# Performance work log

Measured on AMD Instinct MI355X. Metric: run time of the kernel, lower is better.

The kernel has to match this reference:

```python
import jax, jax.numpy as jnp
import numpy as np

N, E, C, NTT, NMOL = 200000, 1600000, 128, 20000, 2000
EPS = 1e-5


def setup_inputs() -> dict:
    key = jax.random.key(0)
    ks = jax.random.split(key, 32)
    s = 0.05
    d = {}
    d["node_attr"] = jax.random.normal(ks[0], (N, C), jnp.float32)
    d["adj_index"] = jax.random.randint(ks[1], (2, E), 0, N)
    d["adj_value"] = jax.random.uniform(ks[2], (E,), jnp.float32)
    d["tt_node_batch"] = jnp.sort(jax.random.randint(ks[3], (N,), 0, NTT))
    d["tt_graph_batch"] = jnp.sort(jax.random.randint(ks[4], (NTT,), 0, NMOL))
    # GCN layers (2): linear weight/bias
    d["W_gcn"] = jax.random.normal(ks[5], (2, C, C)) * s
    d["b_gcn"] = jnp.zeros((2, C))
    # 8 BatchNorm1d(C): [gcn0, gcn1, tt0, tt1, tt2, mol0, mol1, mol2] (eval mode)
    d["bn_gamma"] = jnp.ones((8, C))
    d["bn_beta"] = jnp.zeros((8, C))
    d["bn_mean"] = jnp.zeros((8, C))
    d["bn_var"] = jnp.ones((8, C))
    # 2 GATConv (tt, mol): bipartite lin_src/lin_dst, att_src/att_dst, bias (heads=1)
    d["gat_Wsrc"] = jax.random.normal(ks[6], (2, C, C)) * s
    d["gat_Wdst"] = jax.random.normal(ks[7], (2, C, C)) * s
    d["gat_asrc"] = jax.random.normal(ks[8], (2, C)) * s
    d["gat_adst"] = jax.random.normal(ks[9], (2, C)) * s
    d["gat_bias"] = jnp.zeros((2, C))
    # 2 GRUCell(C, C)
    d["gru_Wih"] = jax.random.normal(ks[10], (2, 3 * C, C)) * s
    d["gru_Whh"] = jax.random.normal(ks[11], (2, 3 * C, C)) * s
    d["gru_bih"] = jnp.zeros((2, 3 * C))
    d["gru_bhh"] = jnp.zeros((2, 3 * C))
    # predictor: 128 -> 64 (relu) -> 1
    d["pW1"] = jax.random.normal(ks[12], (64, C)) * s
    d["pb1"] = jnp.full((64,), 0.01)
    d["pW2"] = jax.random.normal(ks[13], (1, 64)) * s
    d["pb2"] = jnp.full((1,), 0.01)
    return d


def _bn(x, i, g, b, m, v):
    return (x - m[i]) * (g[i] / jnp.sqrt(v[i] + EPS)) + b[i]


def _spmm(idx, val, x, n):  # out[i] = sum_j A[i,j] x[j]
    return jax.ops.segment_sum(val[:, None] * x[idx[1]], idx[0], num_segments=n)


def _gat(x_src, x_dst, src, dst, nseg, Ws, Wd, a_s, a_d, bias):
    hs = x_src @ Ws.T
    hd = x_dst @ Wd.T
    alpha = jax.nn.leaky_relu(hs @ a_s, 0.01 * 0 + 0.01) if False else None
    a = (hs @ a_s)[src] + (hd @ a_d)[dst]
    a = jnp.where(a > 0, a, 0.01 * a)  # leaky_relu, negative_slope=0.01
    mx = jax.ops.segment_max(a, dst, num_segments=nseg)
    e = jnp.exp(a - mx[dst])
    den = jax.ops.segment_sum(e, dst, num_segments=nseg)
    w = e / den[dst]
    return jax.ops.segment_sum(w[:, None] * hs[src], dst, num_segments=nseg) + bias


def _gru(x, h, Wih, Whh, bih, bhh):
    gi = x @ Wih.T + bih
    gh = h @ Whh.T + bhh
    ir, iz, inn = jnp.split(gi, 3, axis=-1)
    hr, hz, hn = jnp.split(gh, 3, axis=-1)
    r = jax.nn.sigmoid(ir + hr)
    z = jax.nn.sigmoid(iz + hz)
    n = jnp.tanh(inn + r * hn)
    return (1.0 - z) * n + z * h


def _pool_stage(x, seg, nseg, bn_base, gi, bn_gamma, bn_beta, bn_mean, bn_var,
                gat_Wsrc, gat_Wdst, gat_asrc, gat_adst, gat_bias,
                gru_Wih, gru_Whh, gru_bih, gru_bhh):
    x = _bn(x, bn_base, bn_gamma, bn_beta, bn_mean, bn_var)
    mean = jax.ops.segment_sum(x, seg, num_segments=nseg)  # global_add_pool
    mean = _bn(jax.nn.relu(mean), bn_base + 1, bn_gamma, bn_beta, bn_mean, bn_var)
    src = jnp.arange(x.shape[0])
    g = _gat(x, mean, src, seg, nseg, gat_Wsrc[gi], gat_Wdst[gi], gat_asrc[gi], gat_adst[gi], gat_bias[gi])
    g = jax.nn.elu(g)  # dropout p=0.001 is identity in eval
    g = _gru(g, mean, gru_Wih[gi], gru_Whh[gi], gru_bih[gi], gru_bhh[gi])
    return _bn(jax.nn.relu(g), bn_base + 2, bn_gamma, bn_beta, bn_mean, bn_var)


def reference(node_attr, adj_value, W_gcn, b_gcn, bn_gamma, bn_beta, bn_mean, bn_var,
              gat_Wsrc, gat_Wdst, gat_asrc, gat_adst, gat_bias,
              gru_Wih, gru_Whh, gru_bih, gru_bhh, pW1, pb1, pW2, pb2,
              adj_index, tt_node_batch, tt_graph_batch):
    # graph embedder: two GCN layers  x <- relu(BN(A @ (x W^T) + b))
    x = node_attr
    for i in range(2):
        x = _spmm(adj_index, adj_value, x @ W_gcn[i].T, N) + b_gcn[i]
        x = jax.nn.relu(_bn(x, i, bn_gamma, bn_beta, bn_mean, bn_var))
    # tt pooling: nodes -> tt subgraphs
    tt = _pool_stage(x, tt_node_batch, NTT, 2, 0, bn_gamma, bn_beta, bn_mean, bn_var,
                     gat_Wsrc, gat_Wdst, gat_asrc, gat_adst, gat_bias,
                     gru_Wih, gru_Whh, gru_bih, gru_bhh)
    # mol pooling: tt subgraphs -> molecules
    mol = _pool_stage(tt, tt_graph_batch, NMOL, 5, 1, bn_gamma, bn_beta, bn_mean, bn_var,
                      gat_Wsrc, gat_Wdst, gat_asrc, gat_adst, gat_bias,
                      gru_Wih, gru_Whh, gru_bih, gru_bhh)
    # predictor
    h = jax.nn.relu(mol @ pW1.T + pb1)
    return h @ pW2.T + pb2  # [NMOL, 1]
```

## Files before the change

### kernel.cpp

```cpp
#include <hip/hip_runtime.h>
#include <math.h>

#define CCH 128
#define G3  384
#define BN_EPS 1e-5f
#define BSH 9
#define BROWS 512
#define COLBITS 19

typedef __bf16 bf16;
typedef __bf16 bf16x2 __attribute__((ext_vector_type(2)));
typedef __bf16 bf16x4 __attribute__((ext_vector_type(4)));
typedef __bf16 bf16x8 __attribute__((ext_vector_type(8)));
typedef float f32x4 __attribute__((ext_vector_type(4)));

__global__ __launch_bounds__(256) void prep_kernel(
    const float* __restrict__ g, const float* __restrict__ b,
    const float* __restrict__ m, const float* __restrict__ v,
    float* __restrict__ bnsc, float* __restrict__ bnsh,
    const float* __restrict__ Wsrc, const float* __restrict__ Wdst,
    const float* __restrict__ asrc, const float* __restrict__ adst,
    float* __restrict__ vsp, float* __restrict__ vd, float* __restrict__ c0,
    const int* __restrict__ tt_node_batch, int N, int NTT, int* __restrict__ starts_tt,
    const int* __restrict__ tt_graph_batch, int NMOL, int* __restrict__ starts_mol,
    int* __restrict__ bhist,
    const float* __restrict__ Wgcn, bf16* __restrict__ Wgcnb,
    bf16* __restrict__ Wsrcb,
    const float* __restrict__ Wih, bf16* __restrict__ Wihb,
    const float* __restrict__ Whh, bf16* __restrict__ Whhb,
    int B1, int B2, int B3, int B4, int B5, int B6, int B7, int B8)
{
    __shared__ float red[2];
    const int bid = blockIdx.x;
    const int tid = threadIdx.x;
    if (bid < B1) {
        int idx = bid * 256 + tid;
        if (idx < 8 * CCH) {
            float s = g[idx] / sqrtf(v[idx] + BN_EPS);
            bnsc[idx] = s;
            bnsh[idx] = b[idx] - m[idx] * s;
        }
    } else if (bid < B2) {
        int s = bid - B1;
        int which = tid >> 7, k = tid & 127;
        const float* W = (which ? Wdst : Wsrc) + s * CCH * CCH;
        const float* a = (which ? adst : asrc) + s * CCH;
        float acc = 0.f;
        for (int j = 0; j < CCH; ++j) acc += W[j * CCH + k] * a[j];
        if (which) {
            vd[s * CCH + k] = acc;
        } else {
            int l = 2 + 3 * s;
            float scl = g[l * CCH + k] / sqrtf(v[l * CCH + k] + BN_EPS);
            float shf = b[l * CCH + k] - m[l * CCH + k] * scl;
            vsp[s * CCH + k] = acc * scl;
            float p = shf * acc;
            for (int o = 32; o; o >>= 1) p += __shfl_down(p, o);
            if ((k & 63) == 0) red[k >> 6] = p;
        }
        __syncthreads();
        if (tid == 0) c0[s] = red[0] + red[1];
    } else if (bid < B3) {
        int s = (bid - B2) * 256 + tid;
        if (s <= NTT) {
            int lo = 0, hi = N;
            while (lo < hi) { int mid = (lo + hi) >> 1; if (tt_node_batch[mid] < s) lo = mid + 1; else hi = mid; }
            starts_tt[s] = lo;
        }
    } else if (bid < B4) {
        int s = (bid - B3) * 256 + tid;
        if (s <= NMOL) {
            int lo = 0, hi = NTT;
            while (lo < hi) { int mid = (lo + hi) >> 1; if (tt_graph_batch[mid] < s) lo = mid + 1; else hi = mid; }
            starts_mol[s] = lo;
        }
    } else if (bid < B5) {
        bhist[tid] = 0; bhist[tid + 256] = 0;
    } else {
        const float* src; bf16* dst; int u0;
        if (bid < B6)      { src = Wgcn; dst = Wgcnb; u0 = (bid - B5) * 256; }
        else if (bid < B7) { src = Wsrc; dst = Wsrcb; u0 = (bid - B6) * 256; }
        else if (bid < B8) { src = Wih;  dst = Wihb;  u0 = (bid - B7) * 256; }
        else               { src = Whh;  dst = Whhb;  u0 = (bid - B8) * 256; }
        int u = u0 + tid;
        int row = u >> 4, kc = u & 15;
        int bi = row >> 7, nrow = row & 127;
        const float* s = src + (size_t)row * CCH + kc * 8;
        float4 a = *(const float4*)s;
        float4 b4 = *(const float4*)(s + 4);
        bf16x8 o = { (bf16)a.x, (bf16)a.y, (bf16)a.z, (bf16)a.w,
                     (bf16)b4.x, (bf16)b4.y, (bf16)b4.z, (bf16)b4.w };
        *(bf16x8*)&dst[(size_t)bi * 16384 + ((kc * 128 + nrow) << 3)] = o;
    }
}


__global__ __launch_bounds__(256) void bucket_hist_kernel(const int* __restrict__ rows,
                                                          int* __restrict__ bhist, int E)
{
    __shared__ int h[512];
    int t = threadIdx.x;
    h[t] = 0; h[t + 256] = 0;
    __syncthreads();
    int base = blockIdx.x * 4096;
#pragma unroll
    for (int i = 0; i < 16; ++i) {
        int e = base + i * 256 + t;
        if (e < E) atomicAdd(&h[rows[e] >> BSH], 1);
    }
    __syncthreads();
    if (h[t]) atomicAdd(&bhist[t], h[t]);
    if (h[t + 256]) atomicAdd(&bhist[t + 256], h[t + 256]);
}

__global__ __launch_bounds__(256) void bucket_scan_kernel(const int* __restrict__ bhist,
                                                          int* __restrict__ boff, int* __restrict__ bcur,
                                                          int* __restrict__ row_ptr, int NB, int N, int E)
{
    __shared__ int h[512], sx[512], wt[4];
    int t = threadIdx.x;
    h[t] = bhist[t]; h[t + 256] = bhist[t + 256];
    __syncthreads();
    int v0 = h[2 * t], v1 = h[2 * t + 1];
    int s = v0 + v1, incl = s;
    for (int o = 1; o < 64; o <<= 1) { int u = __shfl_up(incl, o); if ((t & 63) >= o) incl += u; }
    if ((t & 63) == 63) wt[t >> 6] = incl;
    __syncthreads();
    int woff = 0, w = t >> 6;
    for (int i = 0; i < w; ++i) woff += wt[i];
    int excl = woff + incl - s;
    sx[2 * t] = excl; sx[2 * t + 1] = excl + v0;
    __syncthreads();
    if (t < NB)       { boff[t] = sx[t];       bcur[t] = sx[t]; }
    if (t + 256 < NB) { boff[t + 256] = sx[t + 256]; bcur[t + 256] = sx[t + 256]; }
    if (t == 0) { boff[NB] = E; row_ptr[N] = E; }
}

__global__ __launch_bounds__(256) void bucket_bin_kernel(
    const int* __restrict__ rows, const int* __restrict__ cols, const float* __restrict__ val,
    int* __restrict__ bcur, int2* __restrict__ bcv, int E)
{
    __shared__ int hist[512], sx[512], cnt[512], gbase[512], wt[4];
    __shared__ int mb[4096];
    __shared__ int2 mcv[4096];
    int t = threadIdx.x;
    hist[t] = 0; hist[t + 256] = 0; cnt[t] = 0; cnt[t + 256] = 0;
    __syncthreads();
    int base = blockIdx.x * 4096;
    int r[16];
#pragma unroll
    for (int i = 0; i < 16; ++i) {
        int e = base + i * 256 + t;
        r[i] = (e < E) ? rows[e] : -1;
        if (r[i] >= 0) atomicAdd(&hist[r[i] >> BSH], 1);
    }
    __syncthreads();
    int v0 = hist[2 * t], v1 = hist[2 * t + 1];
    int s = v0 + v1, incl = s;
    for (int o = 1; o < 64; o <<= 1) { int u = __shfl_up(incl, o); if ((t & 63) >= o) incl += u; }
    if ((t & 63) == 63) wt[t >> 6] = incl;
    __syncthreads();
    int woff = 0, w = t >> 6;
    for (int i = 0; i < w; ++i) woff += wt[i];
    int excl = woff + incl - s;
    sx[2 * t] = excl; sx[2 * t + 1] = excl + v0;
    __syncthreads();
    for (int bb = t; bb < 512; bb += 256)
        if (hist[bb]) gbase[bb] = atomicAdd(&bcur[bb], hist[bb]);
    __syncthreads();
#pragma unroll
    for (int i = 0; i < 16; ++i) {
        if (r[i] < 0) continue;
        int e = base + i * 256 + t;
        int bb = r[i] >> BSH;
        int p = atomicAdd(&cnt[bb], 1);
        int loc = sx[bb] + p;
        mb[loc] = bb;
        int2 cv;
        cv.x = cols[e] | ((r[i] & (BROWS - 1)) << COLBITS);
        cv.y = __float_as_int(val[e]);
        mcv[loc] = cv;
    }
    __syncthreads();
    int Mv = sx[511] + hist[511];
    for (int loc = t; loc < Mv; loc += 256) {
        int bb = mb[loc];
        int gidx = gbase[bb] + (loc - sx[bb]);
        bcv[gidx] = mcv[loc];
    }
}

__global__ __launch_bounds__(256) void bucket_place_kernel(
    const int2* __restrict__ bcv, const int* __restrict__ boff, int* __restrict__ row_ptr,
    int2* __restrict__ cpack, int N)
{
    __shared__ int rcnt[512], sx[512], wt[4];
    int b = blockIdx.x;
    int t = threadIdx.x;
    rcnt[t] = 0; rcnt[t + 256] = 0;
    __syncthreads();
    int rbase = b << BSH;
    int rn = min(BROWS, N - rbase);
    int lo = boff[b], hi = boff[b + 1];
    for (int p = lo + t; p < hi; p += 256)
        atomicAdd(&rcnt[((unsigned)bcv[p].x) >> COLBITS], 1);
    __syncthreads();
    int v0 = rcnt[2 * t], v1 = rcnt[2 * t + 1];
    int s = v0 + v1, incl = s;
    for (int o = 1; o < 64; o <<= 1) { int u = __shfl_up(incl, o); if ((t & 63) >= o) incl += u; }
    if ((t & 63) == 63) wt[t >> 6] = incl;
    __syncthreads();
    int woff = 0, w = t >> 6;
    for (int i = 0; i < w; ++i) woff += wt[i];
    int excl = woff + incl - s;
    sx[2 * t] = excl; sx[2 * t + 1] = excl + v0;
    __syncthreads();
    if (t < rn)       row_ptr[rbase + t] = lo + sx[t];
    if (t + 256 < rn) row_ptr[rbase + t + 256] = lo + sx[t + 256];
    __syncthreads();
    sx[t] += lo; sx[t + 256] += lo;
    __syncthreads();
    for (int p = lo + t; p < hi; p += 256) {
        int2 cv = bcv[p];
        int rin = ((unsigned)cv.x) >> COLBITS;
        int slot = atomicAdd(&sx[rin], 1);
        cv.x &= (1 << COLBITS) - 1;
        cpack[slot] = cv;
    }
}

template<int IN_BF16, int OUT_BF16, int ACT>
__global__ __launch_bounds__(256, 4) void gemm_mfma(
    const void* __restrict__ Xv, const bf16* __restrict__ Wf,
    const float* __restrict__ bias, void* __restrict__ Yv, int M, int Nout)
{
    __shared__ bf16 Xs[128 * 128];
    const int tid = threadIdx.x;
    const int rb = blockIdx.x * 128;
    const int cb = blockIdx.y * 128;
    const bf16* Wfb = Wf + (size_t)cb * CCH;

    if (IN_BF16) {
#pragma unroll
        for (int i = 0; i < 8; ++i) {
            int c = tid + i * 256;
            int r = c >> 4, kc = c & 15;
            int grow = rb + r;
            bf16x8 o = {};
            if (grow < M) o = *(const bf16x8*)&((const bf16*)Xv)[(size_t)grow * CCH + kc * 8];
            *(bf16x8*)&Xs[(r * 16 + (kc ^ (r & 15))) << 3] = o;
        }
    } else {
#pragma unroll
        for (int i = 0; i < 16; ++i) {
            int c = tid + i * 256;
            int r = c >> 5, sub = c & 31;
            int kc = sub >> 1, half = sub & 1;
            int grow = rb + r;
            bf16x4 o = {};
            if (grow < M) {
                float4 xv = *(const float4*)&((const float*)Xv)[(size_t)grow * CCH + kc * 8 + half * 4];
                o[0] = (bf16)xv.x; o[1] = (bf16)xv.y; o[2] = (bf16)xv.z; o[3] = (bf16)xv.w;
            }
            *(bf16x4*)&Xs[((r * 16 + (kc ^ (r & 15))) << 3) + half * 4] = o;
        }
    }
    __syncthreads();

    const int w = tid >> 6, lane = tid & 63;
    const int col16 = lane & 15, quad = lane >> 4;
    const int wm = (w & 1) * 64, wn = (w >> 1) * 64;

    f32x4 acc[4][4] = {};
#pragma unroll
    for (int kk = 0; kk < 4; ++kk) {
        const int kc = kk * 4 + quad;
        bf16x8 bfr[4], af[4];
#pragma unroll
        for (int ni = 0; ni < 4; ++ni)
            bfr[ni] = *(const bf16x8*)&Wfb[(size_t)((kc * 128 + wn + ni * 16 + col16) << 3)];
#pragma unroll
        for (int mi = 0; mi < 4; ++mi) {
            int r = wm + mi * 16 + col16;
            af[mi] = *(const bf16x8*)&Xs[(r * 16 + (kc ^ col16)) << 3];
        }
#pragma unroll
        for (int mi = 0; mi < 4; ++mi)
#pragma unroll
            for (int ni = 0; ni < 4; ++ni)
                acc[mi][ni] = __builtin_amdgcn_mfma_f32_16x16x32_bf16(af[mi], bfr[ni], acc[mi][ni], 0, 0, 0);
    }

#pragma unroll
    for (int mi = 0; mi < 4; ++mi) {
#pragma unroll
        for (int r = 0; r < 4; ++r) {
            int row = rb + wm + mi * 16 + quad * 4 + r;
            if (row >= M) continue;
#pragma unroll
            for (int ni = 0; ni < 4; ++ni) {
                int col = cb + wn + ni * 16 + col16;
                float vv = acc[mi][ni][r];
                if (bias) vv += bias[col];
                if (ACT == 1) vv = vv > 0.f ? vv : expm1f(vv);
                if (OUT_BF16) ((bf16*)Yv)[(size_t)row * Nout + col] = (bf16)vv;
                else          ((float*)Yv)[(size_t)row * Nout + col] = vv;
            }
        }
    }
}

template<int TT>
__global__ __launch_bounds__(256, 2) void gru_gemm_kernel(
    const bf16* __restrict__ Agi, const float* __restrict__ meanf,
    const bf16* __restrict__ Wih, const bf16* __restrict__ Whh,
    const float* __restrict__ bih, const float* __restrict__ bhh,
    const float* __restrict__ sc4, const float* __restrict__ sh4,
    void* __restrict__ out,
    const float* __restrict__ vsp2, const float* __restrict__ c02, float* __restrict__ scores,
    int M)
{
    __shared__ bf16 Xi[32 * 128];
    __shared__ bf16 Xh[32 * 128];
    __shared__ float sred[32];
    const int tid = threadIdx.x;
    const int rb = blockIdx.x * 32;

    if (TT && tid < 32) sred[tid] = 0.f;
#pragma unroll
    for (int i = 0; i < 2; ++i) {
        int c = tid + i * 256;
        int r = c >> 4, kc = c & 15;
        int grow = rb + r;
        bf16x8 o = {};
        if (grow < M) o = *(const bf16x8*)&Agi[(size_t)grow * CCH + kc * 8];
        *(bf16x8*)&Xi[(r * 16 + (kc ^ (r & 15))) << 3] = o;
    }
#pragma unroll
    for (int i = 0; i < 4; ++i) {
        int c = tid + i * 256;
        int r = c >> 5, sub = c & 31;
        int kc = sub >> 1, half = sub & 1;
        int grow = rb + r;
        bf16x4 o = {};
        if (grow < M) {
            float4 xv = *(const float4*)&meanf[(size_t)grow * CCH + kc * 8 + half * 4];
            o[0] = (bf16)xv.x; o[1] = (bf16)xv.y; o[2] = (bf16)xv.z; o[3] = (bf16)xv.w;
        }
        *(bf16x4*)&Xh[((r * 16 + (kc ^ (r & 15))) << 3) + half * 4] = o;
    }
    __syncthreads();

    const int w = tid >> 6, lane = tid & 63;
    const int col16 = lane & 15, quad = lane >> 4;

    f32x4 carry[2][2];

    const int phase_cb[3] = {0, 2, 1};
#pragma unroll
    for (int ph = 0; ph < 3; ++ph) {
        const int cb = phase_cb[ph];
        const bf16* Wi_t = Wih + (size_t)cb * 16384;
        const bf16* Wh_t = Whh + (size_t)cb * 16384;
        f32x4 ai[2][2] = {};
        f32x4 ah[2][2] = {};
#pragma unroll
        for (int kk = 0; kk < 4; ++kk) {
            const int kc = kk * 4 + quad;
            bf16x8 bi_f[2], bh_f[2], xi_f[2], xh_f[2];
#pragma unroll
            for (int ni = 0; ni < 2; ++ni) {
                int wc = w * 32 + ni * 16 + col16;
                bi_f[ni] = *(const bf16x8*)&Wi_t[(size_t)((kc * 128 + wc) << 3)];
                bh_f[ni] = *(const bf16x8*)&Wh_t[(size_t)((kc * 128 + wc) << 3)];
            }
#pragma unroll
            for (int mi = 0; mi < 2; ++mi) {
                int r = mi * 16 + col16;
                xi_f[mi] = *(const bf16x8*)&Xi[(r * 16 + (kc ^ col16)) << 3];
                xh_f[mi] = *(const bf16x8*)&Xh[(r * 16 + (kc ^ col16)) << 3];
            }
#pragma unroll
            for (int mi = 0; mi < 2; ++mi)
#pragma unroll
                for (int ni = 0; ni < 2; ++ni) {
                    ai[mi][ni] = __builtin_amdgcn_mfma_f32_16x16x32_bf16(xi_f[mi], bi_f[ni], ai[mi][ni], 0, 0, 0);
                    ah[mi][ni] = __builtin_amdgcn_mfma_f32_16x16x32_bf16(xh_f[mi], bh_f[ni], ah[mi][ni], 0, 0, 0);
                }
        }
        const int gofs = cb * 128;
#pragma unroll
        for (int mi = 0; mi < 2; ++mi) {
#pragma unroll
            for (int ni = 0; ni < 2; ++ni) {
                int col = w * 32 + ni * 16 + col16;
                float bi_v = bih[gofs + col], bh_v = bhh[gofs + col];
#pragma unroll
                for (int rr = 0; rr < 4; ++rr) {
                    float vi = ai[mi][ni][rr] + bi_v;
                    float vh = ah[mi][ni][rr] + bh_v;
                    if (ph == 0) {
                        carry[mi][ni][rr] = 1.f / (1.f + __expf(-(vi + vh)));
                    } else if (ph == 1) {
                        carry[mi][ni][rr] = tanhf(vi + carry[mi][ni][rr] * vh);
                    } else {
                        float z = 1.f / (1.f + __expf(-(vi + vh)));
                        int row = rb + mi * 16 + quad * 4 + rr;
                        float mval = (row < M) ? meanf[(size_t)row * CCH + col] : 0.f;
                        float h = (1.f - z) * carry[mi][ni][rr] + z * mval;
                        h = fmaxf(h, 0.f);
                        carry[mi][ni][rr] = h * sc4[col] + sh4[col];
                    }
                }
            }
        }
    }

#pragma unroll
    for (int mi = 0; mi < 2; ++mi) {
#pragma unroll
        for (int rr = 0; rr < 4; ++rr) {
            int rloc = mi * 16 + quad * 4 + rr;
            int row = rb + rloc;
            float p = 0.f;
#pragma unroll
            for (int ni = 0; ni < 2; ++ni) {
                int col = w * 32 + ni * 16 + col16;
                float o = carry[mi][ni][rr];
                if (row < M) {
                    if (TT) ((bf16*)out)[(size_t)row * CCH + col] = (bf16)o;
                    else    ((float*)out)[(size_t)row * CCH + col] = o;
                }
                if (TT) p += o * vsp2[col];
            }
            if (TT && row < M) atomicAdd(&sred[rloc], p);
        }
    }
    if (TT) {
        __syncthreads();
        if (tid < 32 && rb + tid < M) scores[rb + tid] = sred[tid] + c02[0];
    }
}

template<int SCORES>
__global__ __launch_bounds__(256) void spmm_csr_kernel(
    const int* __restrict__ row_ptr, const int2* __restrict__ cpack,
    const bf16* __restrict__ Xin, bf16* __restrict__ Y,
    const float* __restrict__ bvec, const float* __restrict__ sc, const float* __restrict__ sh,
    const float* __restrict__ vsp, const float* __restrict__ c0p, float* __restrict__ scores,
    int Nrow)
{
    int gid = blockIdx.x * 256 + threadIdx.x;
    int row = gid >> 4;
    if (row >= Nrow) return;
    int l8 = (gid & 15) << 3;
    int st = row_ptr[row], en = row_ptr[row + 1];
    float acc[8] = {};
    int j = st;
    for (; j + 4 <= en; j += 4) {
        int2 p0 = cpack[j], p1 = cpack[j + 1], p2 = cpack[j + 2], p3 = cpack[j + 3];
        bf16x8 x0 = *(const bf16x8*)&Xin[(size_t)p0.x * CCH + l8];
        bf16x8 x1 = *(const bf16x8*)&Xin[(size_t)p1.x * CCH + l8];
        bf16x8 x2 = *(const bf16x8*)&Xin[(size_t)p2.x * CCH + l8];
        bf16x8 x3 = *(const bf16x8*)&Xin[(size_t)p3.x * CCH + l8];
        float v0 = __int_as_float(p0.y), v1 = __int_as_float(p1.y);
        float v2 = __int_as_float(p2.y), v3 = __int_as_float(p3.y);
#pragma unroll
        for (int q = 0; q < 8; ++q)
            acc[q] += v0 * (float)x0[q] + v1 * (float)x1[q] + v2 * (float)x2[q] + v3 * (float)x3[q];
    }
    if (j + 2 <= en) {
        int2 p0 = cpack[j], p1 = cpack[j + 1];
        bf16x8 x0 = *(const bf16x8*)&Xin[(size_t)p0.x * CCH + l8];
        bf16x8 x1 = *(const bf16x8*)&Xin[(size_t)p1.x * CCH + l8];
        float v0 = __int_as_float(p0.y), v1 = __int_as_float(p1.y);
#pragma unroll
        for (int q = 0; q < 8; ++q) acc[q] += v0 * (float)x0[q] + v1 * (float)x1[q];
        j += 2;
    }
    if (j < en) {
        int2 p0 = cpack[j];
        bf16x8 x0 = *(const bf16x8*)&Xin[(size_t)p0.x * CCH + l8];
        float v0 = __int_as_float(p0.y);
#pragma unroll
        for (int q = 0; q < 8; ++q) acc[q] += v0 * (float)x0[q];
    }
    float o[8];
    bf16x8 ov;
#pragma unroll
    for (int q = 0; q < 8; ++q) {
        o[q] = fmaxf((acc[q] + bvec[l8 + q]) * sc[l8 + q] + sh[l8 + q], 0.f);
        ov[q] = (bf16)o[q];
    }
    *(bf16x8*)&Y[(size_t)row * CCH + l8] = ov;
    if (SCORES) {
        float p = 0.f;
#pragma unroll
        for (int q = 0; q < 8; ++q) p += o[q] * vsp[l8 + q];
        for (int d = 8; d; d >>= 1) p += __shfl_down(p, d, 16);
        if ((gid & 15) == 0) scores[row] = p + c0p[0];
    }
}

__global__ __launch_bounds__(128) void segstage_kernel(
    const bf16* __restrict__ X, const float* __restrict__ sarr, const int* __restrict__ starts,
    const float* __restrict__ sc2, const float* __restrict__ sh2,
    const float* __restrict__ sc3, const float* __restrict__ sh3,
    const float* __restrict__ vd, float* __restrict__ mean, bf16* __restrict__ upool)
{
    __shared__ float red[2];
    __shared__ float adsh;
    int t = blockIdx.x;
    int c = threadIdx.x;
    int st = starts[t], en = starts[t + 1];
    float sum = 0.f;
    for (int i = st; i < en; ++i) sum += (float)X[(size_t)i * CCH + c];
    float cnt = (float)(en - st);
    float poolb = fmaxf(sum * sc2[c] + cnt * sh2[c], 0.f);
    float mv = poolb * sc3[c] + sh3[c];
    mean[(size_t)t * CCH + c] = mv;
    float p = mv * vd[c];
    for (int o = 32; o; o >>= 1) p += __shfl_down(p, o);
    if ((c & 63) == 0) red[c >> 6] = p;
    __syncthreads();
    if (c == 0) adsh = red[0] + red[1];
    __syncthreads();
    if (en == st) { upool[(size_t)t * CCH + c] = (bf16)0.f; return; }
    float adt = adsh;
    float lm = -3.0e38f;
    for (int i = st + c; i < en; i += 128) {
        float a = sarr[i] + adt;
        a = a > 0.f ? a : 0.01f * a;
        lm = fmaxf(lm, a);
    }
    for (int o = 32; o; o >>= 1) lm = fmaxf(lm, __shfl_down(lm, o));
    if ((c & 63) == 0) red[c >> 6] = lm;
    __syncthreads();
    float m = fmaxf(red[0], red[1]);
    float u = 0.f, den = 0.f;
    for (int i = st; i < en; ++i) {
        float a = sarr[i] + adt;
        a = a > 0.f ? a : 0.01f * a;
        float e = __expf(a - m);
        den += e;
        u += e * (float)X[(size_t)i * CCH + c];
    }
    upool[(size_t)t * CCH + c] = (bf16)((u / den) * sc2[c] + sh2[c]);
}

__global__ __launch_bounds__(64) void pred_kernel(
    const float* __restrict__ mol, const float* __restrict__ pW1, const float* __restrict__ pb1,
    const float* __restrict__ pW2, const float* __restrict__ pb2, float* __restrict__ out)
{
    __shared__ float row[CCH];
    int m = blockIdx.x;
    int j = threadIdx.x;
    row[j] = mol[(size_t)m * CCH + j];
    row[j + 64] = mol[(size_t)m * CCH + 64 + j];
    __syncthreads();
    float h = pb1[j];
#pragma unroll
    for (int k = 0; k < CCH; ++k) h += row[k] * pW1[j * CCH + k];
    h = fmaxf(h, 0.f);
    float p = h * pW2[j];
    for (int o = 32; o; o >>= 1) p += __shfl_down(p, o);
    if (j == 0) out[m] = p + pb2[0];
}


extern "C" void kernel_launch(void* const* d_in, const int* in_sizes, int n_in,
                              void* d_out, int out_size, void* d_ws, size_t ws_size,
                              hipStream_t stream)
{
    (void)n_in; (void)ws_size;
    const float* node_attr      = (const float*)d_in[0];
    const int*   adj_index      = (const int*)  d_in[1];
    const float* adj_value      = (const float*)d_in[2];
    const int*   tt_node_batch  = (const int*)  d_in[3];
    const int*   tt_graph_batch = (const int*)  d_in[4];
    const float* W_gcn    = (const float*)d_in[5];
    const float* b_gcn    = (const float*)d_in[6];
    const float* bn_gamma = (const float*)d_in[7];
    const float* bn_beta  = (const float*)d_in[8];
    const float* bn_mean  = (const float*)d_in[9];
    const float* bn_var   = (const float*)d_in[10];
    const float* gat_Wsrc = (const float*)d_in[11];
    const float* gat_Wdst = (const float*)d_in[12];
    const float* gat_asrc = (const float*)d_in[13];
    const float* gat_adst = (const float*)d_in[14];
    const float* gat_bias = (const float*)d_in[15];
    const float* gru_Wih  = (const float*)d_in[16];
    const float* gru_Whh  = (const float*)d_in[17];
    const float* gru_bih  = (const float*)d_in[18];
    const float* gru_bhh  = (const float*)d_in[19];
    const float* pW1 = (const float*)d_in[20];
    const float* pb1 = (const float*)d_in[21];
    const float* pW2 = (const float*)d_in[22];
    const float* pb2 = (const float*)d_in[23];

    const int E    = in_sizes[2];
    const int N    = in_sizes[3];
    const int NTT  = in_sizes[4];
    const int NMOL = out_size;
    const int NB   = (N + BROWS - 1) >> BSH;

    const int* adj_rows = adj_index;
    const int* adj_cols = adj_index + E;

    char* wsb = (char*)d_ws;
    size_t off = 0;
    auto carve = [&](size_t bytes) -> char* {
        char* p = wsb + off;
        off = (off + bytes + 255) & ~(size_t)255;
        return p;
    };
    bf16* bufB = (bf16*)carve((size_t)N * CCH * 2);
    bf16* bufA = (bf16*)carve((size_t)N * CCH * 2);
    bf16* tt   = (bf16*)carve((size_t)NTT * CCH * 2);
    float* mol  = (float*)carve((size_t)NMOL * CCH * 4);
    float* mean  = (float*)carve((size_t)NTT * CCH * 4);
    bf16*  upool = (bf16*)carve((size_t)NTT * CCH * 2);
    bf16*  gbuf  = (bf16*)carve((size_t)NTT * CCH * 2);
    float* scores = (float*)carve((size_t)N * 4);
    int* starts_tt  = (int*)carve((size_t)(NTT + 1) * 4);
    int* starts_mol = (int*)carve((size_t)(NMOL + 1) * 4);
    float* bnsc = (float*)carve(8 * CCH * 4);
    float* bnsh = (float*)carve(8 * CCH * 4);
    float* vsp  = (float*)carve(2 * CCH * 4);
    float* vd   = (float*)carve(2 * CCH * 4);
    float* c0   = (float*)carve(2 * 4);
    bf16* Wgcnb = (bf16*)carve((size_t)2 * CCH * CCH * 2);
    bf16* Wsrcb = (bf16*)carve((size_t)2 * CCH * CCH * 2);
    bf16* Wihb  = (bf16*)carve((size_t)2 * G3 * CCH * 2);
    bf16* Whhb  = (bf16*)carve((size_t)2 * G3 * CCH * 2);
    int*   bhist   = (int*)carve(512 * 4);
    int*   boff    = (int*)carve((size_t)(NB + 1) * 4);
    int*   bcur    = (int*)carve((size_t)NB * 4);
    int*   row_ptr = (int*)carve((size_t)(N + 1) * 4);
    int2*  bcv     = (int2*)carve((size_t)E * 8);
    int2*  cpack   = (int2*)carve((size_t)E * 8);

    const int B1 = 4;
    const int B2 = B1 + 2;
    const int B3 = B2 + (NTT + 1 + 255) / 256;
    const int B4 = B3 + (NMOL + 1 + 255) / 256;
    const int B5 = B4 + 1;
    const int B6 = B5 + 16;
    const int B7 = B6 + 16;
    const int B8 = B7 + 48;
    const int B9 = B8 + 48;
    prep_kernel<<<B9, 256, 0, stream>>>(
        bn_gamma, bn_beta, bn_mean, bn_var, bnsc, bnsh,
        gat_Wsrc, gat_Wdst, gat_asrc, gat_adst, vsp, vd, c0,
        tt_node_batch, N, NTT, starts_tt,
        tt_graph_batch, NMOL, starts_mol,
        bhist,
        W_gcn, Wgcnb, Wsrcb, gru_Wih, Wihb, gru_Whh, Whhb,
        B1, B2, B3, B4, B5, B6, B7, B8);

    const int nchunk = (E + 4095) / 4096;
    bucket_hist_kernel<<<nchunk, 256, 0, stream>>>(adj_rows, bhist, E);
    bucket_scan_kernel<<<1, 256, 0, stream>>>(bhist, boff, bcur, row_ptr, NB, N, E);
    bucket_bin_kernel<<<nchunk, 256, 0, stream>>>(adj_rows, adj_cols, adj_value, bcur, bcv, E);
    bucket_place_kernel<<<NB, 256, 0, stream>>>(bcv, boff, row_ptr, cpack, N);

    dim3 gg((N + 127) / 128, 1);
    const int spmm_blocks = ((size_t)N * 16 + 255) / 256;
    gemm_mfma<0, 1, 0><<<gg, 256, 0, stream>>>(node_attr, Wgcnb, nullptr, bufB, N, CCH);
    spmm_csr_kernel<0><<<spmm_blocks, 256, 0, stream>>>(
        row_ptr, cpack, bufB, bufA, b_gcn, bnsc, bnsh, nullptr, nullptr, nullptr, N);
    gemm_mfma<1, 1, 0><<<gg, 256, 0, stream>>>(bufA, Wgcnb + CCH * CCH, nullptr, bufB, N, CCH);
    spmm_csr_kernel<1><<<spmm_blocks, 256, 0, stream>>>(
        row_ptr, cpack, bufB, bufA, b_gcn + CCH, bnsc + CCH, bnsh + CCH,
        vsp, c0, scores, N);

    {
        const int bnb = 2, gi = 0, nseg = NTT;
        segstage_kernel<<<nseg, 128, 0, stream>>>(bufA, scores, starts_tt,
            bnsc + bnb * CCH, bnsh + bnb * CCH, bnsc + (bnb + 1) * CCH, bnsh + (bnb + 1) * CCH,
            vd + gi * CCH, mean, upool);
        dim3 g1((nseg + 127) / 128, 1);
        gemm_mfma<1, 1, 1><<<g1, 256, 0, stream>>>(upool, Wsrcb + gi * CCH * CCH,
                                                   gat_bias + gi * CCH, gbuf, nseg, CCH);
        gru_gemm_kernel<1><<<(nseg + 31) / 32, 256, 0, stream>>>(
            gbuf, mean, Wihb + gi * G3 * CCH, Whhb + gi * G3 * CCH,
            gru_bih + gi * G3, gru_bhh + gi * G3,
            bnsc + (bnb + 2) * CCH, bnsh + (bnb + 2) * CCH,
            tt, vsp + CCH, c0 + 1, scores, nseg);
    }

    {
        const int bnb = 5, gi = 1, nseg = NMOL;
        segstage_kernel<<<nseg, 128, 0, stream>>>(tt, scores, starts_mol,
            bnsc + bnb * CCH, bnsh + bnb * CCH, bnsc + (bnb + 1) * CCH, bnsh + (bnb + 1) * CCH,
            vd + gi * CCH, mean, upool);
        dim3 g1((nseg + 127) / 128, 1);
        gemm_mfma<1, 1, 1><<<g1, 256, 0, stream>>>(upool, Wsrcb + gi * CCH * CCH,
                                                   gat_bias + gi * CCH, gbuf, nseg, CCH);
        gru_gemm_kernel<0><<<(nseg + 31) / 32, 256, 0, stream>>>(
            gbuf, mean, Wihb + gi * G3 * CCH, Whhb + gi * G3 * CCH,
            gru_bih + gi * G3, gru_bhh + gi * G3,
            bnsc + (bnb + 2) * CCH, bnsh + (bnb + 2) * CCH,
            mol, nullptr, nullptr, nullptr, nseg);
        pred_kernel<<<NMOL, 64, 0, stream>>>(mol, pW1, pb1, pW2, pb2, (float*)d_out);
    }
}
```

Measured before the change: 586.2 us.

## Fuse bucket histogram into prep, predictor into GRU, cache segment rows in LDS

Several independent changes. The edge-row histogram moves into the prep kernel (with a memset replacing the zeroing block), and the predictor MLP is fused into the final GRU kernel, which drops two launches and the mol buffer round-trip. Binning chunks shrink from 4096 to 2048 edges, and bucket placement runs with 512 threads, one row per thread. The segment-pooling kernel caches up to 96 rows per segment in LDS so the softmax-weighted sum does not reread global memory. The trade-off is higher LDS use, which may lower occupancy in segstage, and a predictor loop inside the GRU kernel that runs 8 outputs per thread serially.

```diff
diff --git a/kernel.cpp b/kernel.cpp
--- a/kernel.cpp
+++ b/kernel.cpp
@@ -7,6 +7,8 @@
 #define BSH 9
 #define BROWS 512
 #define COLBITS 19
+#define ECH 2048
+#define SEGC 96
 
 typedef __bf16 bf16;
 typedef __bf16 bf16x2 __attribute__((ext_vector_type(2)));
@@ -23,7 +25,7 @@
     float* __restrict__ vsp, float* __restrict__ vd, float* __restrict__ c0,
     const int* __restrict__ tt_node_batch, int N, int NTT, int* __restrict__ starts_tt,
     const int* __restrict__ tt_graph_batch, int NMOL, int* __restrict__ starts_mol,
-    int* __restrict__ bhist,
+    const int* __restrict__ rows, int E, int* __restrict__ bhist,
     const float* __restrict__ Wgcn, bf16* __restrict__ Wgcnb,
     bf16* __restrict__ Wsrcb,
     const float* __restrict__ Wih, bf16* __restrict__ Wihb,
@@ -31,6 +33,7 @@
     int B1, int B2, int B3, int B4, int B5, int B6, int B7, int B8)
 {
     __shared__ float red[2];
+    __shared__ int h[512];
     const int bid = blockIdx.x;
     const int tid = threadIdx.x;
     if (bid < B1) {
@@ -74,14 +77,12 @@
             while (lo < hi) { int mid = (lo + hi) >> 1; if (tt_graph_batch[mid] < s) lo = mid + 1; else hi = mid; }
             starts_mol[s] = lo;
         }
-    } else if (bid < B5) {
-        bhist[tid] = 0; bhist[tid + 256] = 0;
-    } else {
+    } else if (bid < B8) {
         const float* src; bf16* dst; int u0;
-        if (bid < B6)      { src = Wgcn; dst = Wgcnb; u0 = (bid - B5) * 256; }
-        else if (bid < B7) { src = Wsrc; dst = Wsrcb; u0 = (bid - B6) * 256; }
-        else if (bid < B8) { src = Wih;  dst = Wihb;  u0 = (bid - B7) * 256; }
-        else               { src = Whh;  dst = Whhb;  u0 = (bid - B8) * 256; }
+        if (bid < B5)      { src = Wgcn; dst = Wgcnb; u0 = (bid - B4) * 256; }
+        else if (bid < B6) { src = Wsrc; dst = Wsrcb; u0 = (bid - B5) * 256; }
+        else if (bid < B7) { src = Wih;  dst = Wihb;  u0 = (bid - B6) * 256; }
+        else               { src = Whh;  dst = Whhb;  u0 = (bid - B7) * 256; }
         int u = u0 + tid;
         int row = u >> 4, kc = u & 15;
         int bi = row >> 7, nrow = row & 127;
@@ -91,27 +92,21 @@
         bf16x8 o = { (bf16)a.x, (bf16)a.y, (bf16)a.z, (bf16)a.w,
                      (bf16)b4.x, (bf16)b4.y, (bf16)b4.z, (bf16)b4.w };
         *(bf16x8*)&dst[(size_t)bi * 16384 + ((kc * 128 + nrow) << 3)] = o;
-    }
-}
-
-
-__global__ __launch_bounds__(256) void bucket_hist_kernel(const int* __restrict__ rows,
-                                                          int* __restrict__ bhist, int E)
-{
-    __shared__ int h[512];
-    int t = threadIdx.x;
-    h[t] = 0; h[t + 256] = 0;
-    __syncthreads();
-    int base = blockIdx.x * 4096;
-#pragma unroll
-    for (int i = 0; i < 16; ++i) {
-        int e = base + i * 256 + t;
-        if (e < E) atomicAdd(&h[rows[e] >> BSH], 1);
-    }
-    __syncthreads();
-    if (h[t]) atomicAdd(&bhist[t], h[t]);
-    if (h[t + 256]) atomicAdd(&bhist[t + 256], h[t + 256]);
-}
+    } else {
+        h[tid] = 0; h[tid + 256] = 0;
+        __syncthreads();
+        int base = (bid - B8) * ECH;
+#pragma unroll
+        for (int i = 0; i < ECH / 256; ++i) {
+            int e = base + i * 256 + tid;
+            if (e < E) atomicAdd(&h[rows[e] >> BSH], 1);
+        }
+        __syncthreads();
+        if (h[tid]) atomicAdd(&bhist[tid], h[tid]);
+        if (h[tid + 256]) atomicAdd(&bhist[tid + 256], h[tid + 256]);
+    }
+}
+
 
 __global__ __launch_bounds__(256) void bucket_scan_kernel(const int* __restrict__ bhist,
                                                           int* __restrict__ boff, int* __restrict__ bcur,
@@ -141,15 +136,15 @@
     int* __restrict__ bcur, int2* __restrict__ bcv, int E)
 {
     __shared__ int hist[512], sx[512], cnt[512], gbase[512], wt[4];
-    __shared__ int mb[4096];
-    __shared__ int2 mcv[4096];
+    __shared__ int mb[ECH];
+    __shared__ int2 mcv[ECH];
     int t = threadIdx.x;
     hist[t] = 0; hist[t + 256] = 0; cnt[t] = 0; cnt[t + 256] = 0;
     __syncthreads();
-    int base = blockIdx.x * 4096;
-    int r[16];
-#pragma unroll
-    for (int i = 0; i < 16; ++i) {
+    int base = blockIdx.x * ECH;
+    int r[ECH / 256];
+#pragma unroll
+    for (int i = 0; i < ECH / 256; ++i) {
         int e = base + i * 256 + t;
         r[i] = (e < E) ? rows[e] : -1;
         if (r[i] >= 0) atomicAdd(&hist[r[i] >> BSH], 1);
@@ -169,7 +164,7 @@
         if (hist[bb]) gbase[bb] = atomicAdd(&bcur[bb], hist[bb]);
     __syncthreads();
 #pragma unroll
-    for (int i = 0; i < 16; ++i) {
+    for (int i = 0; i < ECH / 256; ++i) {
         if (r[i] < 0) continue;
         int e = base + i * 256 + t;
         int bb = r[i] >> BSH;
@@ -190,37 +185,33 @@
     }
 }
 
-__global__ __launch_bounds__(256) void bucket_place_kernel(
+__global__ __launch_bounds__(512) void bucket_place_kernel(
     const int2* __restrict__ bcv, const int* __restrict__ boff, int* __restrict__ row_ptr,
     int2* __restrict__ cpack, int N)
 {
-    __shared__ int rcnt[512], sx[512], wt[4];
+    __shared__ int rcnt[512], sx[512], wt[8];
     int b = blockIdx.x;
     int t = threadIdx.x;
-    rcnt[t] = 0; rcnt[t + 256] = 0;
+    rcnt[t] = 0;
     __syncthreads();
     int rbase = b << BSH;
     int rn = min(BROWS, N - rbase);
     int lo = boff[b], hi = boff[b + 1];
-    for (int p = lo + t; p < hi; p += 256)
+    for (int p = lo + t; p < hi; p += 512)
         atomicAdd(&rcnt[((unsigned)bcv[p].x) >> COLBITS], 1);
     __syncthreads();
-    int v0 = rcnt[2 * t], v1 = rcnt[2 * t + 1];
-    int s = v0 + v1, incl = s;
+    int vv = rcnt[t];
+    int incl = vv;
     for (int o = 1; o < 64; o <<= 1) { int u = __shfl_up(incl, o); if ((t & 63) >= o) incl += u; }
     if ((t & 63) == 63) wt[t >> 6] = incl;
     __syncthreads();
     int woff = 0, w = t >> 6;
     for (int i = 0; i < w; ++i) woff += wt[i];
-    int excl = woff + incl - s;
-    sx[2 * t] = excl; sx[2 * t + 1] = excl + v0;
-    __syncthreads();
-    if (t < rn)       row_ptr[rbase + t] = lo + sx[t];
-    if (t + 256 < rn) row_ptr[rbase + t + 256] = lo + sx[t + 256];
-    __syncthreads();
-    sx[t] += lo; sx[t + 256] += lo;
-    __syncthreads();
-    for (int p = lo + t; p < hi; p += 256) {
+    int excl = woff + incl - vv;
+    if (t < rn) row_ptr[rbase + t] = lo + excl;
+    sx[t] = lo + excl;
+    __syncthreads();
+    for (int p = lo + t; p < hi; p += 512) {
         int2 cv = bcv[p];
         int rin = ((unsigned)cv.x) >> COLBITS;
         int slot = atomicAdd(&sx[rin], 1);
@@ -318,11 +309,14 @@
     const float* __restrict__ sc4, const float* __restrict__ sh4,
     void* __restrict__ out,
     const float* __restrict__ vsp2, const float* __restrict__ c02, float* __restrict__ scores,
+    const float* __restrict__ pW1, const float* __restrict__ pb1,
+    const float* __restrict__ pW2, const float* __restrict__ pb2,
     int M)
 {
     __shared__ bf16 Xi[32 * 128];
     __shared__ bf16 Xh[32 * 128];
-    __shared__ float sred[32];
+    __shared__ float sred[TT ? 32 : 1];
+    __shared__ float rowbuf[TT ? 1 : 32 * 132];
     const int tid = threadIdx.x;
     const int rb = blockIdx.x * 32;
 
@@ -416,29 +410,55 @@
         }
     }
 
-#pragma unroll
-    for (int mi = 0; mi < 2; ++mi) {
-#pragma unroll
-        for (int rr = 0; rr < 4; ++rr) {
-            int rloc = mi * 16 + quad * 4 + rr;
-            int row = rb + rloc;
-            float p = 0.f;
-#pragma unroll
-            for (int ni = 0; ni < 2; ++ni) {
-                int col = w * 32 + ni * 16 + col16;
-                float o = carry[mi][ni][rr];
-                if (row < M) {
-                    if (TT) ((bf16*)out)[(size_t)row * CCH + col] = (bf16)o;
-                    else    ((float*)out)[(size_t)row * CCH + col] = o;
+    if (TT) {
+#pragma unroll
+        for (int mi = 0; mi < 2; ++mi) {
+#pragma unroll
+            for (int rr = 0; rr < 4; ++rr) {
+                int rloc = mi * 16 + quad * 4 + rr;
+                int row = rb + rloc;
+                float p = 0.f;
+#pragma unroll
+                for (int ni = 0; ni < 2; ++ni) {
+                    int col = w * 32 + ni * 16 + col16;
+                    float o = carry[mi][ni][rr];
+                    if (row < M) ((bf16*)out)[(size_t)row * CCH + col] = (bf16)o;
+                    p += o * vsp2[col];
                 }
-                if (TT) p += o * vsp2[col];
+                if (row < M) atomicAdd(&sred[rloc], p);
             }
-            if (TT && row < M) atomicAdd(&sred[rloc], p);
-        }
-    }
-    if (TT) {
+        }
         __syncthreads();
         if (tid < 32 && rb + tid < M) scores[rb + tid] = sred[tid] + c02[0];
+    } else {
+#pragma unroll
+        for (int mi = 0; mi < 2; ++mi)
+#pragma unroll
+            for (int rr = 0; rr < 4; ++rr) {
+                int rloc = mi * 16 + quad * 4 + rr;
+#pragma unroll
+                for (int ni = 0; ni < 2; ++ni) {
+                    int col = w * 32 + ni * 16 + col16;
+                    rowbuf[rloc * 132 + col] = carry[mi][ni][rr];
+                }
+            }
+        __syncthreads();
+        int row = tid >> 3;
+        int j0 = (tid & 7) * 8;
+        int grow = rb + row;
+        if (grow < M) {
+            float p = 0.f;
+#pragma unroll
+            for (int jj = 0; jj < 8; ++jj) {
+                int j = j0 + jj;
+                float h = pb1[j];
+                for (int k = 0; k < CCH; ++k) h += rowbuf[row * 132 + k] * pW1[j * CCH + k];
+                h = fmaxf(h, 0.f);
+                p += h * pW2[j];
+            }
+            for (int d = 4; d; d >>= 1) p += __shfl_down(p, d, 8);
+            if ((tid & 7) == 0) ((float*)out)[grow] = p + pb2[0];
+        }
     }
 }
 
@@ -508,14 +528,22 @@
     const float* __restrict__ sc3, const float* __restrict__ sh3,
     const float* __restrict__ vd, float* __restrict__ mean, bf16* __restrict__ upool)
 {
+    __shared__ bf16 xc[SEGC * CCH];
     __shared__ float red[2];
     __shared__ float adsh;
     int t = blockIdx.x;
     int c = threadIdx.x;
     int st = starts[t], en = starts[t + 1];
+    int n = en - st;
+    int nc = n < SEGC ? n : SEGC;
     float sum = 0.f;
-    for (int i = st; i < en; ++i) sum += (float)X[(size_t)i * CCH + c];
-    float cnt = (float)(en - st);
+    for (int i = 0; i < nc; ++i) {
+        bf16 xv = X[(size_t)(st + i) * CCH + c];
+        xc[i * CCH + c] = xv;
+        sum += (float)xv;
+    }
+    for (int i = nc; i < n; ++i) sum += (float)X[(size_t)(st + i) * CCH + c];
+    float cnt = (float)n;
     float poolb = fmaxf(sum * sc2[c] + cnt * sh2[c], 0.f);
     float mv = poolb * sc3[c] + sh3[c];
     mean[(size_t)t * CCH + c] = mv;
@@ -525,7 +553,7 @@
     __syncthreads();
     if (c == 0) adsh = red[0] + red[1];
     __syncthreads();
-    if (en == st) { upool[(size_t)t * CCH + c] = (bf16)0.f; return; }
+    if (n == 0) { upool[(size_t)t * CCH + c] = (bf16)0.f; return; }
     float adt = adsh;
     float lm = -3.0e38f;
     for (int i = st + c; i < en; i += 128) {
@@ -538,33 +566,21 @@
     __syncthreads();
     float m = fmaxf(red[0], red[1]);
     float u = 0.f, den = 0.f;
-    for (int i = st; i < en; ++i) {
-        float a = sarr[i] + adt;
+    for (int i = 0; i < nc; ++i) {
+        float a = sarr[st + i] + adt;
         a = a > 0.f ? a : 0.01f * a;
         float e = __expf(a - m);
         den += e;
-        u += e * (float)X[(size_t)i * CCH + c];
+        u += e * (float)xc[i * CCH + c];
+    }
+    for (int i = nc; i < n; ++i) {
+        float a = sarr[st + i] + adt;
+        a = a > 0.f ? a : 0.01f * a;
+        float e = __expf(a - m);
+        den += e;
+        u += e * (float)X[(size_t)(st + i) * CCH + c];
     }
     upool[(size_t)t * CCH + c] = (bf16)((u / den) * sc2[c] + sh2[c]);
-}
-
-__global__ __launch_bounds__(64) void pred_kernel(
-    const float* __restrict__ mol, const float* __restrict__ pW1, const float* __restrict__ pb1,
-    const float* __restrict__ pW2, const float* __restrict__ pb2, float* __restrict__ out)
-{
-    __shared__ float row[CCH];
-    int m = blockIdx.x;
-    int j = threadIdx.x;
-    row[j] = mol[(size_t)m * CCH + j];
-    row[j + 64] = mol[(size_t)m * CCH + 64 + j];
-    __syncthreads();
-    float h = pb1[j];
-#pragma unroll
-    for (int k = 0; k < CCH; ++k) h += row[k] * pW1[j * CCH + k];
-    h = fmaxf(h, 0.f);
-    float p = h * pW2[j];
-    for (int o = 32; o; o >>= 1) p += __shfl_down(p, o);
-    if (j == 0) out[m] = p + pb2[0];
 }
 
 
@@ -617,7 +633,6 @@
     bf16* bufB = (bf16*)carve((size_t)N * CCH * 2);
     bf16* bufA = (bf16*)carve((size_t)N * CCH * 2);
     bf16* tt   = (bf16*)carve((size_t)NTT * CCH * 2);
-    float* mol  = (float*)carve((size_t)NMOL * CCH * 4);
     float* mean  = (float*)carve((size_t)NTT * CCH * 4);
     bf16*  upool = (bf16*)carve((size_t)NTT * CCH * 2);
     bf16*  gbuf  = (bf16*)carve((size_t)NTT * CCH * 2);
@@ -640,29 +655,29 @@
     int2*  bcv     = (int2*)carve((size_t)E * 8);
     int2*  cpack   = (int2*)carve((size_t)E * 8);
 
+    const int nchunk = (E + ECH - 1) / ECH;
     const int B1 = 4;
     const int B2 = B1 + 2;
     const int B3 = B2 + (NTT + 1 + 255) / 256;
     const int B4 = B3 + (NMOL + 1 + 255) / 256;
-    const int B5 = B4 + 1;
+    const int B5 = B4 + 16;
     const int B6 = B5 + 16;
-    const int B7 = B6 + 16;
+    const int B7 = B6 + 48;
     const int B8 = B7 + 48;
-    const int B9 = B8 + 48;
+    const int B9 = B8 + nchunk;
+    hipMemsetAsync(bhist, 0, 512 * 4, stream);
     prep_kernel<<<B9, 256, 0, stream>>>(
         bn_gamma, bn_beta, bn_mean, bn_var, bnsc, bnsh,
         gat_Wsrc, gat_Wdst, gat_asrc, gat_adst, vsp, vd, c0,
         tt_node_batch, N, NTT, starts_tt,
         tt_graph_batch, NMOL, starts_mol,
-        bhist,
+        adj_rows, E, bhist,
         W_gcn, Wgcnb, Wsrcb, gru_Wih, Wihb, gru_Whh, Whhb,
         B1, B2, B3, B4, B5, B6, B7, B8);
 
-    const int nchunk = (E + 4095) / 4096;
-    bucket_hist_kernel<<<nchunk, 256, 0, stream>>>(adj_rows, bhist, E);
     bucket_scan_kernel<<<1, 256, 0, stream>>>(bhist, boff, bcur, row_ptr, NB, N, E);
     bucket_bin_kernel<<<nchunk, 256, 0, stream>>>(adj_rows, adj_cols, adj_value, bcur, bcv, E);
-    bucket_place_kernel<<<NB, 256, 0, stream>>>(bcv, boff, row_ptr, cpack, N);
+    bucket_place_kernel<<<NB, 512, 0, stream>>>(bcv, boff, row_ptr, cpack, N);
 
     dim3 gg((N + 127) / 128, 1);
     const int spmm_blocks = ((size_t)N * 16 + 255) / 256;
@@ -686,7 +701,8 @@
             gbuf, mean, Wihb + gi * G3 * CCH, Whhb + gi * G3 * CCH,
             gru_bih + gi * G3, gru_bhh + gi * G3,
             bnsc + (bnb + 2) * CCH, bnsh + (bnb + 2) * CCH,
-            tt, vsp + CCH, c0 + 1, scores, nseg);
+            tt, vsp + CCH, c0 + 1, scores,
+            nullptr, nullptr, nullptr, nullptr, nseg);
     }
 
     {
@@ -701,7 +717,7 @@
             gbuf, mean, Wihb + gi * G3 * CCH, Whhb + gi * G3 * CCH,
             gru_bih + gi * G3, gru_bhh + gi * G3,
             bnsc + (bnb + 2) * CCH, bnsh + (bnb + 2) * CCH,
-            mol, nullptr, nullptr, nullptr, nseg);
-        pred_kernel<<<NMOL, 64, 0, stream>>>(mol, pW1, pb1, pW2, pb2, (float*)d_out);
-    }
-}
+            d_out, nullptr, nullptr, nullptr,
+            pW1, pb1, pW2, pb2, nseg);
+    }
+}
```

After: 618.7 us. 1.06x slower.
